# Performance work log

Hardware: AMD Instinct MI355X
Metric: run time of the kernel (lower is better)

The kernel has to match this reference:

```python
import jax, jax.numpy as jnp
import numpy as np

N, F, D, K = 4096, 128, 64, 2  # nodes, in_dim, out_dim, hops


def setup_inputs() -> dict:
    key = jax.random.key(0)
    k_x, k_a, k_e, k_w = jax.random.split(key, 4)
    X = jax.random.normal(k_x, (N, F), jnp.float32)
    # K+1 non-negative dense adjacency/distance matrices (stacked list)
    A = jax.random.uniform(k_a, (K + 1, N, N), jnp.float32)
    # Dense(out_dim, use_bias=False) weights, glorot-like scale
    W_emb = jax.random.normal(k_e, (F, D), jnp.float32) / np.sqrt(F)
    W_hops = jax.random.normal(k_w, (K + 1, F, D), jnp.float32) / np.sqrt(F)
    alpha = jnp.float32(0.1)
    return {"X": X, "A": A, "W_emb": W_emb, "W_hops": W_hops, "alpha": alpha}


def reference(X, A, W_emb, W_hops, alpha):
    # learned embeddings E = Dense(X)  -> [N, D]
    E = X @ W_emb
    # shared low-rank update alpha * E @ E^T  -> [N, N]
    low_rank = alpha * (E @ E.T)
    # per-hop kernel projections Dense_k(X)  -> [K+1, N, D]
    XW = jnp.einsum('nf,kfd->knd', X, W_hops)
    out = jnp.zeros((N, D), X.dtype)
    for k in range(A.shape[0]):  # fixed small K+1 hops
        A_hat = A[k] + low_rank                       # [N, N]
        deg = jnp.sum(A_hat, axis=1)                  # row sums
        d = jnp.power(deg, -0.5)                      # D^{-1/2}
        # D^{-1/2} A_hat D^{-1/2} via broadcast scaling (same math as diag matmuls)
        A_norm = d[:, None] * A_hat * d[None, :]
        out = out + A_norm @ XW[k]
    return jax.nn.relu(out)
```

## Files before the change

### kernel.cpp

```cpp
#include <hip/hip_runtime.h>
#include <math.h>

#define N_ 4096
#define F_ 128
#define D_ 64
#define KH_ 3
#define ZS_ 16
#define KC_ (N_ / ZS_)
#define BM_ 256

#define OFF_E      0
#define OFF_XW     (N_*D_)
#define OFF_SEP    (OFF_XW + KH_*N_*D_)
#define OFF_T      (OFF_SEP + 64*64)
#define OFF_RS     (OFF_T + KH_*D_*D_)
#define OFF_DVEC   (OFF_RS + KH_*N_)
#define OFF_YT     (OFF_DVEC + KH_*N_)
#define OFF_AY     (OFF_YT + KH_*D_*N_/2)

typedef __attribute__((ext_vector_type(8))) short bf16x8;
typedef __attribute__((ext_vector_type(4))) float f32x4;

static __device__ __forceinline__ unsigned short f2bf(float f) {
  union { float f; unsigned u; } v; v.f = f;
  unsigned r = (v.u + 0x7fffu + ((v.u >> 16) & 1u)) >> 16;
  return (unsigned short)r;
}

static __device__ __forceinline__ uint4 pack8(float4 a, float4 b) {
  union { unsigned short u[8]; uint4 q; } pk;
  pk.u[0] = f2bf(a.x); pk.u[1] = f2bf(a.y); pk.u[2] = f2bf(a.z); pk.u[3] = f2bf(a.w);
  pk.u[4] = f2bf(b.x); pk.u[5] = f2bf(b.y); pk.u[6] = f2bf(b.z); pk.u[7] = f2bf(b.w);
  return pk.q;
}

static __device__ __forceinline__ void gload_lds16(const unsigned short* g,
                                                   unsigned short* l) {
  __builtin_amdgcn_global_load_lds(
      (__attribute__((address_space(1))) unsigned int*)g,
      (__attribute__((address_space(3))) unsigned int*)l, 16, 0, 0);
}

__global__ __launch_bounds__(256) void front_kernel(
    const float* __restrict__ A, const float* __restrict__ X,
    const float* __restrict__ W_emb, const float* __restrict__ W_hops,
    float* __restrict__ ws)
{
  const int t = threadIdx.x;
  if (blockIdx.x >= 256) {
    const int db = blockIdx.x - 256;
    ws[OFF_AY + db * 256 + t] = 0.f;
    int lane = t & 63;
    int wave = t >> 6;
    int row = db * 4 + wave;
    const f32x4* Ar = (const f32x4*)(A + (size_t)row * N_);
    float s = 0.f;
#pragma unroll
    for (int it = 0; it < 8; ++it) {
      f32x4 v0 = Ar[it * 128 + lane * 2 + 0];
      f32x4 v1 = Ar[it * 128 + lane * 2 + 1];
      s += (v0[0] + v0[1]) + (v0[2] + v0[3]) + (v1[0] + v1[1]) + (v1[2] + v1[3]);
    }
#pragma unroll
    for (int off = 32; off > 0; off >>= 1)
      s += __shfl_xor(s, off);
    if (lane == 0) ws[OFF_RS + row] = s;
    return;
  }
  __shared__ __align__(16) float sXT[32][68];
  __shared__ __align__(16) float sW[32][68];
  const int m = blockIdx.x >> 6;
  const int rb = blockIdx.x & 63;
  const int row0 = rb * 64;
  const float* W = (m == 0) ? W_emb : (W_hops + (size_t)(m - 1) * F_ * D_);
  float* out = (m == 0) ? (ws + OFF_E) : (ws + OFF_XW + (size_t)(m - 1) * N_ * D_);
  const int tx = t & 15, ty = t >> 4;
  const int d0 = tx * 4, i0 = ty * 4;
  float acc[4][4] = {};
  for (int fc = 0; fc < F_; fc += 32) {
    {
      int i_l = t >> 3;
      int f_l = (t & 7) * 4;
      for (int r = 0; r < 2; ++r) {
        int i = i_l + r * 32;
        float4 v = *(const float4*)(X + (size_t)(row0 + i) * F_ + fc + f_l);
        sXT[f_l + 0][i] = v.x; sXT[f_l + 1][i] = v.y;
        sXT[f_l + 2][i] = v.z; sXT[f_l + 3][i] = v.w;
      }
      int f2 = t >> 4;
      int d  = (t & 15) * 4;
      for (int r = 0; r < 2; ++r) {
        int f = f2 + r * 16;
        *(float4*)&sW[f][d] = *(const float4*)(W + (size_t)(fc + f) * D_ + d);
      }
    }
    __syncthreads();
#pragma unroll 8
    for (int f = 0; f < 32; ++f) {
      float a[4], b[4];
      *(float4*)a = *(const float4*)&sXT[f][i0];
      *(float4*)b = *(const float4*)&sW[f][d0];
      for (int x = 0; x < 4; ++x)
        for (int y = 0; y < 4; ++y)
          acc[x][y] += a[x] * b[y];
    }
    __syncthreads();
  }
  for (int x = 0; x < 4; ++x)
    *(float4*)(out + (size_t)(row0 + i0 + x) * D_ + d0) = *(float4*)acc[x];
  if (m == 0) {
    float p[4];
    for (int y = 0; y < 4; ++y)
      p[y] = acc[0][y] + acc[1][y] + acc[2][y] + acc[3][y];
    *(float4*)&sXT[ty][d0] = *(float4*)p;
    __syncthreads();
    if (ty < 4) {
      int c = ty * 16 + tx;
      float s = 0.f;
#pragma unroll
      for (int r = 0; r < 16; ++r) s += sXT[r][c];
      ws[OFF_SEP + rb * 64 + c] = s;
    }
    if (rb == 0)
      for (int i = t; i < KH_ * D_ * D_; i += 256) ws[OFF_T + i] = 0.f;
  }
}

__global__ __launch_bounds__(256) void prep_kernel(float* __restrict__ ws,
                                                   const float* __restrict__ alpha_p)
{
  const int k = blockIdx.y;
  const float* XWk = ws + OFF_XW + (size_t)k * N_ * D_;
  const float* E   = ws + OFF_E;
  const float* rs  = ws + OFF_RS + (size_t)k * N_;
  const float alpha = *alpha_p;
  int t = threadIdx.x;

  if (blockIdx.x < 64) {
    const int j0 = blockIdx.x * 64;
    unsigned short* Ytk = (unsigned short*)(ws + OFF_YT) + (size_t)k * D_ * N_;
    __shared__ float sS[64];
    __shared__ float sSp[4][64];
    __shared__ float d_l[64];
    __shared__ __align__(16) float sEy[64][65];
    __shared__ float sT[64][65];
    {
      int wv = t >> 6, ln = t & 63;
      float sp = 0.f;
#pragma unroll
      for (int r = 0; r < 16; ++r) sp += ws[OFF_SEP + (wv * 16 + r) * 64 + ln];
      sSp[wv][ln] = sp;
    }
    {
      int j = t >> 2, c0 = (t & 3) * 16;
      for (int r = 0; r < 4; ++r)
        *(float4*)&sEy[j][c0 + 4 * r] = *(const float4*)(E + (size_t)(j0 + j) * D_ + c0 + 4 * r);
    }
    __syncthreads();
    if (t < 64) sS[t] = sSp[0][t] + sSp[1][t] + sSp[2][t] + sSp[3][t];
    __syncthreads();
    {
      int j = t >> 2, c0 = (t & 3) * 16;
      float dot = 0.f;
#pragma unroll
      for (int c = 0; c < 16; ++c) dot += sEy[j][c0 + c] * sS[c0 + c];
      dot += __shfl_xor(dot, 1);
      dot += __shfl_xor(dot, 2);
      if ((t & 3) == 0) {
        float dv = 1.0f / sqrtf(rs[j0 + j] + alpha * dot);
        d_l[j] = dv;
        ws[OFF_DVEC + (size_t)k * N_ + j0 + j] = dv;
      }
    }
    __syncthreads();
    {
      int j = t >> 2;
      int c0 = (t & 3) * 16;
      float dv = d_l[j];
      for (int r = 0; r < 4; ++r) {
        float4 v = *(const float4*)(XWk + (size_t)(j0 + j) * D_ + c0 + 4 * r);
        sT[c0 + 4 * r + 0][j] = v.x * dv;
        sT[c0 + 4 * r + 1][j] = v.y * dv;
        sT[c0 + 4 * r + 2][j] = v.z * dv;
        sT[c0 + 4 * r + 3][j] = v.w * dv;
      }
    }
    __syncthreads();
    {
      int n = t >> 2;
      int jq = (t & 3) * 16;
      __align__(16) unsigned short buf[16];
#pragma unroll
      for (int i = 0; i < 16; ++i) buf[i] = f2bf(sT[n][jq + i]);
      uint4* dst = (uint4*)(Ytk + (size_t)n * N_ + j0 + jq);
      dst[0] = *(uint4*)&buf[0];
      dst[1] = *(uint4*)&buf[8];
    }
  } else {
    __shared__ float sS2[64];
    __shared__ float sSp2[4][64];
    __shared__ float dl2[128];
    __shared__ __align__(16) float sE[32][68];
    __shared__ __align__(16) float sY[32][68];
    int base0 = (blockIdx.x - 64) * 128;
    {
      int wv = t >> 6, ln = t & 63;
      float sp = 0.f;
#pragma unroll
      for (int r = 0; r < 16; ++r) sp += ws[OFF_SEP + (wv * 16 + r) * 64 + ln];
      sSp2[wv][ln] = sp;
    }
    __syncthreads();
    if (t < 64) sS2[t] = sSp2[0][t] + sSp2[1][t] + sSp2[2][t] + sSp2[3][t];
    __syncthreads();
    {
      int jr2 = t >> 1, h = t & 1;
      float dot = 0.f;
#pragma unroll
      for (int c = 0; c < 32; ++c)
        dot += E[(size_t)(base0 + jr2) * D_ + h * 32 + c] * sS2[h * 32 + c];
      dot += __shfl_xor(dot, 1);
      if (h == 0) dl2[jr2] = 1.0f / sqrtf(rs[base0 + jr2] + alpha * dot);
    }
    __syncthreads();
    int tx = t & 15, ty = t >> 4;
    int d0 = tx * 4, c0 = ty * 4;
    float acc[4][4] = {};
    for (int sub = 0; sub < 4; ++sub) {
      int base = base0 + sub * 32;
      {
        int i_l = t >> 3;
        int c   = (t & 7) * 4;
        float dv = dl2[sub * 32 + i_l];
        for (int r = 0; r < 2; ++r) {
          int col = c + r * 32;
          *(float4*)&sE[i_l][col] = *(const float4*)(E + (size_t)(base + i_l) * D_ + col);
          float4 y = *(const float4*)(XWk + (size_t)(base + i_l) * D_ + col);
          y.x *= dv; y.y *= dv; y.z *= dv; y.w *= dv;
          *(float4*)&sY[i_l][col] = y;
        }
      }
      __syncthreads();
#pragma unroll 8
      for (int i = 0; i < 32; ++i) {
        float c4[4], y4[4];
        *(float4*)c4 = *(const float4*)&sE[i][c0];
        *(float4*)y4 = *(const float4*)&sY[i][d0];
        for (int a = 0; a < 4; ++a)
          for (int b = 0; b < 4; ++b)
            acc[a][b] += c4[a] * y4[b];
      }
      __syncthreads();
    }
    float* Tk = ws + OFF_T + (size_t)k * D_ * D_;
    for (int a = 0; a < 4; ++a)
      for (int b = 0; b < 4; ++b)
        atomicAdd(&Tk[(c0 + a) * D_ + d0 + b], acc[a][b]);
  }
}

__global__ __launch_bounds__(256, 3) void agemm_kernel(
    const float* __restrict__ A, const float* __restrict__ ws,
    float* __restrict__ AY)
{
  const int k = blockIdx.y;
  const int row0 = blockIdx.x * BM_;
  const int kz0 = blockIdx.z * KC_;
  const float* Ak = A + ((size_t)k << 24);
  const unsigned short* Ytk = (const unsigned short*)(ws + OFF_YT) + (size_t)k * D_ * N_;

  __shared__ __align__(16) unsigned short sA[BM_ * 64];
  __shared__ __align__(16) unsigned short sY[64 * 64];

  const int t = threadIdx.x;
  const int lane = t & 63;
  const int w = t >> 6;
  const int m = lane & 15;
  const int q = lane >> 4;
  const int sr = t >> 3;
  const int sc = t & 7;
  const int ar = t >> 2;
  const int ac = t & 3;

  f32x4 acc[4][4];
#pragma unroll
  for (int a = 0; a < 4; ++a)
#pragma unroll
    for (int b = 0; b < 4; ++b) acc[a][b] = (f32x4){0.f, 0.f, 0.f, 0.f};

  for (int kt = 0; kt < KC_; kt += 64) {
#pragma unroll
    for (int j = 0; j < 2; ++j) {
      int r = j * 32 + sr;
      gload_lds16(Ytk + (size_t)r * N_ + (kz0 + kt) + ((sc ^ (r & 7)) << 3),
                  &sY[j * 2048 + t * 8]);
    }
#pragma unroll
    for (int p = 0; p < 4; ++p) {
      int r = p * 64 + ar;
      const float* g = Ak + (size_t)(row0 + r) * N_ + (kz0 + kt) + ac * 16;
      float4 v0 = *(const float4*)(g + 0);
      float4 v1 = *(const float4*)(g + 4);
      float4 v2 = *(const float4*)(g + 8);
      float4 v3 = *(const float4*)(g + 12);
      int ch0 = 2 * ac, ch1 = ch0 + 1;
      *(uint4*)&sA[r * 64 + ((ch0 ^ (r & 7)) << 3)] = pack8(v0, v1);
      *(uint4*)&sA[r * 64 + ((ch1 ^ (r & 7)) << 3)] = pack8(v2, v3);
    }
    __syncthreads();
#pragma unroll
    for (int s = 0; s < 2; ++s) {
      bf16x8 av[4], bv[4];
#pragma unroll
      for (int mr = 0; mr < 4; ++mr) {
        int row = w * 64 + mr * 16 + m;
        av[mr] = *(const bf16x8*)&sA[row * 64 + (((s * 4 + q) ^ (row & 7)) << 3)];
      }
#pragma unroll
      for (int nt = 0; nt < 4; ++nt) {
        int n = nt * 16 + m;
        bv[nt] = *(const bf16x8*)&sY[n * 64 + (((s * 4 + q) ^ (n & 7)) << 3)];
      }
#pragma unroll
      for (int mr = 0; mr < 4; ++mr)
#pragma unroll
        for (int nt = 0; nt < 4; ++nt)
          acc[mr][nt] = __builtin_amdgcn_mfma_f32_16x16x32_bf16(av[mr], bv[nt],
                                                                acc[mr][nt], 0, 0, 0);
    }
    __syncthreads();
  }
#pragma unroll
  for (int mr = 0; mr < 4; ++mr) {
    float* outp = AY + ((size_t)k * N_ + row0 + w * 64 + mr * 16) * D_;
#pragma unroll
    for (int nt = 0; nt < 4; ++nt)
#pragma unroll
      for (int r = 0; r < 4; ++r)
        atomicAdd(&outp[(size_t)(q * 4 + r) * D_ + nt * 16 + m], acc[mr][nt][r]);
  }
}

__global__ __launch_bounds__(256) void epilogue_kernel(
    const float* __restrict__ ws, const float* __restrict__ alpha_p,
    float* __restrict__ out)
{
  int g = blockIdx.x * 256 + threadIdx.x;
  int i = g >> 6, d = g & 63;
  const float* E = ws + OFF_E;
  float alpha = *alpha_p;
  float s = 0.f;
#pragma unroll
  for (int k = 0; k < KH_; ++k) {
    float ay = ws[OFF_AY + ((size_t)k * N_ + i) * D_ + d];
    float lr = 0.f;
    const float* Tk = ws + OFF_T + k * D_ * D_;
#pragma unroll 16
    for (int c = 0; c < D_; ++c)
      lr += E[(size_t)i * D_ + c] * Tk[c * D_ + d];
    s += ws[OFF_DVEC + k * N_ + i] * (ay + alpha * lr);
  }
  out[g] = fmaxf(s, 0.f);
}

extern "C" void kernel_launch(void* const* d_in, const int* in_sizes, int n_in,
                              void* d_out, int out_size, void* d_ws, size_t ws_size,
                              hipStream_t stream) {
  const float* X      = (const float*)d_in[0];
  const float* A      = (const float*)d_in[1];
  const float* W_emb  = (const float*)d_in[2];
  const float* W_hops = (const float*)d_in[3];
  const float* alpha_p= (const float*)d_in[4];
  float* out = (float*)d_out;
  float* ws  = (float*)d_ws;

  front_kernel<<<dim3(256 + KH_ * N_ / 4), 256, 0, stream>>>(A, X, W_emb, W_hops, ws);
  prep_kernel<<<dim3(96, KH_), 256, 0, stream>>>(ws, alpha_p);
  agemm_kernel<<<dim3(N_ / BM_, KH_, ZS_), 256, 0, stream>>>(A, ws, ws + OFF_AY);
  epilogue_kernel<<<dim3(N_ * D_ / 256), 256, 0, stream>>>(ws, alpha_p, out);
}
```

Baseline: 376.8 us.

## Pre-convert A to bf16 during rowsum pass and drop split-K atomics

The rowsum pass now also writes a bf16 copy of each adjacency matrix into workspace, and the GEMM loads that copy straight into LDS with async global-to-LDS loads instead of loading fp32 and converting. Split-K partial results go to separate buffers that the epilogue sums, replacing atomics; tile and split sizes are also changed. This trades an extra 100MB write and a larger workspace for simpler, lower-latency GEMM loading.

```diff
diff --git a/kernel.cpp b/kernel.cpp
--- a/kernel.cpp
+++ b/kernel.cpp
@@ -5,9 +5,9 @@
 #define F_ 128
 #define D_ 64
 #define KH_ 3
-#define ZS_ 16
+#define ZS_ 8
 #define KC_ (N_ / ZS_)
-#define BM_ 256
+#define BM_ 128
 
 #define OFF_E      0
 #define OFF_XW     (N_*D_)
@@ -16,7 +16,8 @@
 #define OFF_RS     (OFF_T + KH_*D_*D_)
 #define OFF_DVEC   (OFF_RS + KH_*N_)
 #define OFF_YT     (OFF_DVEC + KH_*N_)
-#define OFF_AY     (OFF_YT + KH_*D_*N_/2)
+#define OFF_AYP    (OFF_YT + KH_*D_*N_/2)
+#define OFF_ABF    (OFF_AYP + ZS_*KH_*N_*D_)
 
 typedef __attribute__((ext_vector_type(8))) short bf16x8;
 typedef __attribute__((ext_vector_type(4))) float f32x4;
@@ -27,10 +28,10 @@
   return (unsigned short)r;
 }
 
-static __device__ __forceinline__ uint4 pack8(float4 a, float4 b) {
+static __device__ __forceinline__ uint4 pack8v(f32x4 a, f32x4 b) {
   union { unsigned short u[8]; uint4 q; } pk;
-  pk.u[0] = f2bf(a.x); pk.u[1] = f2bf(a.y); pk.u[2] = f2bf(a.z); pk.u[3] = f2bf(a.w);
-  pk.u[4] = f2bf(b.x); pk.u[5] = f2bf(b.y); pk.u[6] = f2bf(b.z); pk.u[7] = f2bf(b.w);
+  pk.u[0] = f2bf(a[0]); pk.u[1] = f2bf(a[1]); pk.u[2] = f2bf(a[2]); pk.u[3] = f2bf(a[3]);
+  pk.u[4] = f2bf(b[0]); pk.u[5] = f2bf(b[1]); pk.u[6] = f2bf(b[2]); pk.u[7] = f2bf(b[3]);
   return pk.q;
 }
 
@@ -49,17 +50,18 @@
   const int t = threadIdx.x;
   if (blockIdx.x >= 256) {
     const int db = blockIdx.x - 256;
-    ws[OFF_AY + db * 256 + t] = 0.f;
     int lane = t & 63;
     int wave = t >> 6;
     int row = db * 4 + wave;
     const f32x4* Ar = (const f32x4*)(A + (size_t)row * N_);
+    unsigned short* Br = (unsigned short*)(ws + OFF_ABF) + (size_t)row * N_;
     float s = 0.f;
 #pragma unroll
     for (int it = 0; it < 8; ++it) {
-      f32x4 v0 = Ar[it * 128 + lane * 2 + 0];
-      f32x4 v1 = Ar[it * 128 + lane * 2 + 1];
+      f32x4 v0 = __builtin_nontemporal_load(Ar + it * 128 + lane * 2 + 0);
+      f32x4 v1 = __builtin_nontemporal_load(Ar + it * 128 + lane * 2 + 1);
       s += (v0[0] + v0[1]) + (v0[2] + v0[3]) + (v1[0] + v1[1]) + (v1[2] + v1[3]);
+      *(uint4*)(Br + (size_t)it * 512 + lane * 8) = pack8v(v0, v1);
     }
 #pragma unroll
     for (int off = 32; off > 0; off >>= 1)
@@ -260,13 +262,12 @@
 }
 
 __global__ __launch_bounds__(256, 3) void agemm_kernel(
-    const float* __restrict__ A, const float* __restrict__ ws,
-    float* __restrict__ AY)
+    const float* __restrict__ ws, float* __restrict__ AYp)
 {
   const int k = blockIdx.y;
   const int row0 = blockIdx.x * BM_;
   const int kz0 = blockIdx.z * KC_;
-  const float* Ak = A + ((size_t)k << 24);
+  const unsigned short* Ak = (const unsigned short*)(ws + OFF_ABF) + ((size_t)k << 24);
   const unsigned short* Ytk = (const unsigned short*)(ws + OFF_YT) + (size_t)k * D_ * N_;
 
   __shared__ __align__(16) unsigned short sA[BM_ * 64];
@@ -279,41 +280,33 @@
   const int q = lane >> 4;
   const int sr = t >> 3;
   const int sc = t & 7;
-  const int ar = t >> 2;
-  const int ac = t & 3;
-
-  f32x4 acc[4][4];
-#pragma unroll
-  for (int a = 0; a < 4; ++a)
+
+  f32x4 acc[2][4];
+#pragma unroll
+  for (int a = 0; a < 2; ++a)
 #pragma unroll
     for (int b = 0; b < 4; ++b) acc[a][b] = (f32x4){0.f, 0.f, 0.f, 0.f};
 
   for (int kt = 0; kt < KC_; kt += 64) {
+#pragma unroll
+    for (int j = 0; j < 4; ++j) {
+      int r = j * 32 + sr;
+      gload_lds16(Ak + (size_t)(row0 + r) * N_ + (kz0 + kt) + ((sc ^ (r & 7)) << 3),
+                  &sA[j * 2048 + t * 8]);
+    }
 #pragma unroll
     for (int j = 0; j < 2; ++j) {
       int r = j * 32 + sr;
       gload_lds16(Ytk + (size_t)r * N_ + (kz0 + kt) + ((sc ^ (r & 7)) << 3),
                   &sY[j * 2048 + t * 8]);
     }
-#pragma unroll
-    for (int p = 0; p < 4; ++p) {
-      int r = p * 64 + ar;
-      const float* g = Ak + (size_t)(row0 + r) * N_ + (kz0 + kt) + ac * 16;
-      float4 v0 = *(const float4*)(g + 0);
-      float4 v1 = *(const float4*)(g + 4);
-      float4 v2 = *(const float4*)(g + 8);
-      float4 v3 = *(const float4*)(g + 12);
-      int ch0 = 2 * ac, ch1 = ch0 + 1;
-      *(uint4*)&sA[r * 64 + ((ch0 ^ (r & 7)) << 3)] = pack8(v0, v1);
-      *(uint4*)&sA[r * 64 + ((ch1 ^ (r & 7)) << 3)] = pack8(v2, v3);
-    }
     __syncthreads();
 #pragma unroll
     for (int s = 0; s < 2; ++s) {
-      bf16x8 av[4], bv[4];
-#pragma unroll
-      for (int mr = 0; mr < 4; ++mr) {
-        int row = w * 64 + mr * 16 + m;
+      bf16x8 av[2], bv[4];
+#pragma unroll
+      for (int mr = 0; mr < 2; ++mr) {
+        int row = w * 32 + mr * 16 + m;
         av[mr] = *(const bf16x8*)&sA[row * 64 + (((s * 4 + q) ^ (row & 7)) << 3)];
       }
 #pragma unroll
@@ -322,7 +315,7 @@
         bv[nt] = *(const bf16x8*)&sY[n * 64 + (((s * 4 + q) ^ (n & 7)) << 3)];
       }
 #pragma unroll
-      for (int mr = 0; mr < 4; ++mr)
+      for (int mr = 0; mr < 2; ++mr)
 #pragma unroll
         for (int nt = 0; nt < 4; ++nt)
           acc[mr][nt] = __builtin_amdgcn_mfma_f32_16x16x32_bf16(av[mr], bv[nt],
@@ -331,13 +324,13 @@
     __syncthreads();
   }
 #pragma unroll
-  for (int mr = 0; mr < 4; ++mr) {
-    float* outp = AY + ((size_t)k * N_ + row0 + w * 64 + mr * 16) * D_;
+  for (int mr = 0; mr < 2; ++mr) {
+    float* outp = AYp + (((size_t)blockIdx.z * KH_ + k) * N_ + row0 + w * 32 + mr * 16) * D_;
 #pragma unroll
     for (int nt = 0; nt < 4; ++nt)
 #pragma unroll
       for (int r = 0; r < 4; ++r)
-        atomicAdd(&outp[(size_t)(q * 4 + r) * D_ + nt * 16 + m], acc[mr][nt][r]);
+        outp[(size_t)(q * 4 + r) * D_ + nt * 16 + m] = acc[mr][nt][r];
   }
 }
 
@@ -352,7 +345,10 @@
   float s = 0.f;
 #pragma unroll
   for (int k = 0; k < KH_; ++k) {
-    float ay = ws[OFF_AY + ((size_t)k * N_ + i) * D_ + d];
+    float ay = 0.f;
+#pragma unroll
+    for (int jc = 0; jc < ZS_; ++jc)
+      ay += ws[OFF_AYP + (((size_t)jc * KH_ + k) * N_ + i) * D_ + d];
     float lr = 0.f;
     const float* Tk = ws + OFF_T + k * D_ * D_;
 #pragma unroll 16
@@ -376,6 +372,6 @@
 
   front_kernel<<<dim3(256 + KH_ * N_ / 4), 256, 0, stream>>>(A, X, W_emb, W_hops, ws);
   prep_kernel<<<dim3(96, KH_), 256, 0, stream>>>(ws, alpha_p);
-  agemm_kernel<<<dim3(N_ / BM_, KH_, ZS_), 256, 0, stream>>>(A, ws, ws + OFF_AY);
+  agemm_kernel<<<dim3(N_ / BM_, KH_, ZS_), 256, 0, stream>>>(ws, ws + OFF_AYP);
   epilogue_kernel<<<dim3(N_ * D_ / 256), 256, 0, stream>>>(ws, alpha_p, out);
 }
```

After: 336.4 us. 10.7% less time.
